# Kernel optimization log

Measured on AMD Instinct MI355X. Metric: run time of the kernel, lower is better.

The kernel has to match this reference:

```python
import jax, jax.numpy as jnp
import numpy as np

NEG_SLOPE = 0.1
K = 3  # kernel_size

def lrelu(x):
    return jnp.where(x >= 0, x, NEG_SLOPE * x)

def setup_inputs() -> dict:
    key = jax.random.key(0)
    ks = jax.random.split(key, 10)
    B, C, H, W = 16, 64, 128, 128
    DEG, RED = 512, 8
    s = 0.02
    return {
        "feat": jax.random.normal(ks[0], (B, C, H, W), jnp.float32),
        "deg": jax.random.normal(ks[1], (B, DEG, 8, 8), jnp.float32),
        # adaptive_size: Linear(deg_fsize -> C), no bias; torch weight [out,in]
        "W_size": jax.random.normal(ks[2], (C, DEG), jnp.float32) * s,
        # kernel net: Linear(C -> C//red), Linear(C//red -> C*K*K)
        "W_k1": jax.random.normal(ks[3], (C // RED, C), jnp.float32) * s,
        "W_k2": jax.random.normal(ks[4], (C * K * K, C // RED), jnp.float32) * s,
        # 1x1 conv C_in -> C_out with bias (stored as [out,in])
        "W_conv": jax.random.normal(ks[5], (C, C), jnp.float32) * s,
        "b_conv": jax.random.normal(ks[6], (C,), jnp.float32) * s,
        # CA layer: 1x1 conv deg_fsize -> C, then C -> C//red -> C
        "W_ac": jax.random.normal(ks[7], (C, DEG), jnp.float32) * s,
        "W_du1": jax.random.normal(ks[8], (C // RED, C), jnp.float32) * s,
        "W_du2": jax.random.normal(ks[9], (C, C // RED), jnp.float32) * s,
    }

def reference(feat, deg, W_size, W_k1, W_k2, W_conv, b_conv, W_ac, W_du1, W_du2):
    b, c, h, w = feat.shape
    # degradation pooled to a vector: AdaptiveAvgPool2d((1,1)) == mean over HW
    dvec = deg.mean(axis=(2, 3))                      # [B, deg_fsize]
    f = dvec @ W_size.T                               # [B, C]
    # per-sample dynamic depthwise kernels
    kern = lrelu(f @ W_k1.T) @ W_k2.T                 # [B, C*K*K]
    kern = kern.reshape(b * c, 1, K, K)               # [B*C, 1, K, K]
    out = jax.lax.conv_general_dilated(
        feat.reshape(1, b * c, h, w), kern,
        window_strides=(1, 1), padding=[((K - 1) // 2,) * 2] * 2,
        feature_group_count=b * c,
        dimension_numbers=("NCHW", "OIHW", "NCHW"))
    out = lrelu(out).reshape(b, c, h, w)
    # trailing 1x1 conv with bias
    out = jnp.einsum("bchw,oc->bohw", out, W_conv) + b_conv[None, :, None, None]
    # CA branch
    fa = dvec @ W_ac.T                                # [B, C]
    att = jax.nn.sigmoid(lrelu(fa @ W_du1.T) @ W_du2.T)  # [B, C_out]
    return out + feat * att[:, :, None, None]
```

## Files before the change

### kernel.cpp

```cpp
#include <hip/hip_runtime.h>
#include <math.h>

#define NEG_SLOPE 0.1f

typedef __attribute__((ext_vector_type(8))) short short8;
typedef __attribute__((ext_vector_type(4))) short short4v;
typedef __attribute__((ext_vector_type(4))) float floatx4;

__device__ __forceinline__ float lrelu(float x) { return x >= 0.0f ? x : NEG_SLOPE * x; }

__device__ __forceinline__ unsigned short f2bf(float x) {
  unsigned u = __float_as_uint(x);
  return (unsigned short)((u + 0x7fffu + ((u >> 16) & 1u)) >> 16);
}

__device__ __forceinline__ float wave_sum64(float v) {
  #pragma unroll
  for (int s = 32; s > 0; s >>= 1) v += __shfl_xor(v, s, 64);
  return v;
}

__global__ __launch_bounds__(256) void prep_dvec(
    const float* __restrict__ deg, float* __restrict__ dvec_ws) {
  const int b = blockIdx.x >> 2;
  const int quarter = blockIdx.x & 3;
  const int t = threadIdx.x;
  const int half = t & 1, row = t >> 1;
  const int d = quarter * 128 + row;
  const float* p = deg + (size_t)b * 32768 + (size_t)d * 64 + half * 32;
  float4 x0 = *(const float4*)(p);
  float4 x1 = *(const float4*)(p + 4);
  float4 x2 = *(const float4*)(p + 8);
  float4 x3 = *(const float4*)(p + 12);
  float4 x4 = *(const float4*)(p + 16);
  float4 x5 = *(const float4*)(p + 20);
  float4 x6 = *(const float4*)(p + 24);
  float4 x7 = *(const float4*)(p + 28);
  float s = (x0.x + x0.y + x0.z + x0.w) + (x1.x + x1.y + x1.z + x1.w) +
            (x2.x + x2.y + x2.z + x2.w) + (x3.x + x3.y + x3.z + x3.w) +
            (x4.x + x4.y + x4.z + x4.w) + (x5.x + x5.y + x5.z + x5.w) +
            (x6.x + x6.y + x6.z + x6.w) + (x7.x + x7.y + x7.z + x7.w);
  s += __shfl_xor(s, 1, 64);
  if (half == 0) dvec_ws[b * 512 + d] = s * (1.0f / 64.0f);
}

__global__ __launch_bounds__(256) void prep_fmul(
    const float* __restrict__ W_size, const float* __restrict__ W_ac,
    const float* __restrict__ dvec_ws, float* __restrict__ f_ws,
    float* __restrict__ fa_ws) {
  const int b = blockIdx.x >> 3;
  const int g = blockIdx.x & 7;
  const int t = threadIdx.x;
  const int dot = t >> 4;
  const int s = t & 15;
  const int c = g * 8 + (dot & 7);
  const float* wr =
      (dot < 8 ? W_size + (size_t)c * 512 : W_ac + (size_t)c * 512) + s * 32;
  const float* dv = dvec_ws + b * 512 + s * 32;
  float p = 0.0f;
  #pragma unroll
  for (int k = 0; k < 8; ++k) {
    float4 w4 = *(const float4*)(wr + k * 4);
    float4 d4 = *(const float4*)(dv + k * 4);
    p += w4.x * d4.x + w4.y * d4.y + w4.z * d4.z + w4.w * d4.w;
  }
  p += __shfl_xor(p, 1, 64);
  p += __shfl_xor(p, 2, 64);
  p += __shfl_xor(p, 4, 64);
  p += __shfl_xor(p, 8, 64);
  if (s == 0) {
    if (dot < 8) f_ws[b * 64 + c] = p;
    else         fa_ws[b * 64 + c] = p;
  }
}

__global__ __launch_bounds__(256) void prep_tail(
    const float* __restrict__ W_k1, const float* __restrict__ W_k2,
    const float* __restrict__ W_du1, const float* __restrict__ W_du2,
    const float* __restrict__ f_ws, const float* __restrict__ fa_ws,
    float* __restrict__ kern_ws, float* __restrict__ att_ws) {
  const int b = blockIdx.x;
  const int t = threadIdx.x;
  __shared__ float t1s[8], t2s[8];
  const int wave = t >> 6, lane = t & 63;
  if (wave == 0) {
    float v = f_ws[b * 64 + lane];
    #pragma unroll
    for (int rr = 0; rr < 8; ++rr) {
      float p = wave_sum64(v * W_k1[rr * 64 + lane]);
      if (lane == 0) t1s[rr] = lrelu(p);
    }
  } else if (wave == 1) {
    float v = fa_ws[b * 64 + lane];
    #pragma unroll
    for (int rr = 0; rr < 8; ++rr) {
      float p = wave_sum64(v * W_du1[rr * 64 + lane]);
      if (lane == 0) t2s[rr] = lrelu(p);
    }
  }
  __syncthreads();

  for (int i = t; i < 576; i += 256) {
    float4 wa0 = *(const float4*)&W_k2[i * 8];
    float4 wa1 = *(const float4*)&W_k2[i * 8 + 4];
    kern_ws[b * 576 + i] =
        t1s[0] * wa0.x + t1s[1] * wa0.y + t1s[2] * wa0.z + t1s[3] * wa0.w +
        t1s[4] * wa1.x + t1s[5] * wa1.y + t1s[6] * wa1.z + t1s[7] * wa1.w;
  }
  if (t < 64) {
    float4 wa0 = *(const float4*)&W_du2[t * 8];
    float4 wa1 = *(const float4*)&W_du2[t * 8 + 4];
    float s = t2s[0] * wa0.x + t2s[1] * wa0.y + t2s[2] * wa0.z + t2s[3] * wa0.w +
              t2s[4] * wa1.x + t2s[5] * wa1.y + t2s[6] * wa1.z + t2s[7] * wa1.w;
    att_ws[b * 64 + t] = 1.0f / (1.0f + expf(-s));
  }
}

__global__ __launch_bounds__(256, 5) void fused_kernel(
    const float* __restrict__ feat, const float* __restrict__ W_conv,
    const float* __restrict__ b_conv, const float* __restrict__ kern_ws,
    const float* __restrict__ att_ws, float* __restrict__ out) {
  const int bid = blockIdx.x;
  const int b = bid >> 7;
  const int h = bid & 127;

  const int t = threadIdx.x;

  __shared__ __align__(16) unsigned short zT[128 * 72];
  __shared__ __align__(16) unsigned short wt[64 * 72];
  __shared__ float ks[576];
  __shared__ float atts[64];
  __shared__ float bcs[64];

  {
    const int o = t >> 2;
    const int c0 = (t & 3) * 16;
    const float* wp = W_conv + o * 64 + c0;
    float4 a0 = *(const float4*)(wp);
    float4 a1 = *(const float4*)(wp + 4);
    float4 a2 = *(const float4*)(wp + 8);
    float4 a3 = *(const float4*)(wp + 12);
    const int sw = ((o >> 2) ^ (o >> 5)) & 7;
    short8 p0, p1;
    p0[0] = f2bf(a0.x); p0[1] = f2bf(a0.y); p0[2] = f2bf(a0.z); p0[3] = f2bf(a0.w);
    p0[4] = f2bf(a1.x); p0[5] = f2bf(a1.y); p0[6] = f2bf(a1.z); p0[7] = f2bf(a1.w);
    p1[0] = f2bf(a2.x); p1[1] = f2bf(a2.y); p1[2] = f2bf(a2.z); p1[3] = f2bf(a2.w);
    p1[4] = f2bf(a3.x); p1[5] = f2bf(a3.y); p1[6] = f2bf(a3.z); p1[7] = f2bf(a3.w);
    const int kc0 = ((c0 >> 3) + 0) ^ sw;
    const int kc1 = ((c0 >> 3) + 1) ^ sw;
    *(short8*)&wt[o * 72 + kc0 * 8] = p0;
    *(short8*)&wt[o * 72 + kc1 * 8] = p1;
  }
  for (int i = t; i < 576; i += 256) ks[i] = kern_ws[b * 576 + i];
  if (t < 64) { atts[t] = att_ws[b * 64 + t]; bcs[t] = b_conv[t]; }
  __syncthreads();

  const size_t base_b = (size_t)b * 64 * 128 * 128;
  const int lane = t & 63, wave = t >> 6;
  const int cq = t >> 5;
  const int gg = t & 31;
  const int w0 = gg * 4;
  const int swz = (gg ^ (gg >> 3)) & 7;
  const float4 zf4 = {0.f, 0.f, 0.f, 0.f};

  const bool hgt0 = (h > 0), hlt = (h < 127);
  const float* fbase = feat + base_b + (size_t)h * 128 + w0;

  #pragma unroll
  for (int it = 0; it < 2; ++it) {
    const int c0 = cq * 4 + it * 32;
    float4 top[4], mid[4], bot[4];
    #pragma unroll
    for (int j = 0; j < 4; ++j) {
      const float* p = fbase + (size_t)(c0 + j) * 16384;
      mid[j] = *(const float4*)p;
      top[j] = hgt0 ? *(const float4*)(p - 128) : zf4;
      bot[j] = hlt  ? *(const float4*)(p + 128) : zf4;
    }
    unsigned short sres[4][4];
    #pragma unroll
    for (int j = 0; j < 4; ++j) {
      const float* kv = &ks[(c0 + j) * 9];
      const float k0 = kv[0], k1 = kv[1], k2 = kv[2];
      const float k3 = kv[3], k4 = kv[4], k5 = kv[5];
      const float k6 = kv[6], k7 = kv[7], k8 = kv[8];
      float a0 = 0.f, a1 = 0.f, a2 = 0.f, a3 = 0.f;
      {
        float4 m = top[j];
        float lf = __shfl(m.w, lane - 1, 64); if (gg == 0)  lf = 0.f;
        float rt = __shfl(m.x, lane + 1, 64); if (gg == 31) rt = 0.f;
        a0 += k0 * lf  + k1 * m.x + k2 * m.y;
        a1 += k0 * m.x + k1 * m.y + k2 * m.z;
        a2 += k0 * m.y + k1 * m.z + k2 * m.w;
        a3 += k0 * m.z + k1 * m.w + k2 * rt;
      }
      {
        float4 m = mid[j];
        float lf = __shfl(m.w, lane - 1, 64); if (gg == 0)  lf = 0.f;
        float rt = __shfl(m.x, lane + 1, 64); if (gg == 31) rt = 0.f;
        a0 += k3 * lf  + k4 * m.x + k5 * m.y;
        a1 += k3 * m.x + k4 * m.y + k5 * m.z;
        a2 += k3 * m.y + k4 * m.z + k5 * m.w;
        a3 += k3 * m.z + k4 * m.w + k5 * rt;
      }
      {
        float4 m = bot[j];
        float lf = __shfl(m.w, lane - 1, 64); if (gg == 0)  lf = 0.f;
        float rt = __shfl(m.x, lane + 1, 64); if (gg == 31) rt = 0.f;
        a0 += k6 * lf  + k7 * m.x + k8 * m.y;
        a1 += k6 * m.x + k7 * m.y + k8 * m.z;
        a2 += k6 * m.y + k7 * m.z + k8 * m.w;
        a3 += k6 * m.z + k7 * m.w + k8 * rt;
      }
      sres[j][0] = f2bf(lrelu(a0));
      sres[j][1] = f2bf(lrelu(a1));
      sres[j][2] = f2bf(lrelu(a2));
      sres[j][3] = f2bf(lrelu(a3));
    }
    const int chunk = (cq >> 1) + it * 4;
    const int kcs = ((chunk ^ swz) * 8) + (cq & 1) * 4;
    #pragma unroll
    for (int i = 0; i < 4; ++i) {
      short4v sv;
      sv[0] = (short)sres[0][i]; sv[1] = (short)sres[1][i];
      sv[2] = (short)sres[2][i]; sv[3] = (short)sres[3][i];
      *(short4v*)&zT[(w0 + i) * 72 + kcs] = sv;
    }
  }
  __syncthreads();

  {
    const int r = lane & 15, q = lane >> 4;

    short8 az[2][2];
    #pragma unroll
    for (int wm2 = 0; wm2 < 2; ++wm2) {
      const int w = (wave * 2 + wm2) * 16 + r;
      const int sz = ((w >> 2) ^ (w >> 5)) & 7;
      #pragma unroll
      for (int ksp = 0; ksp < 2; ++ksp) {
        const int kc = (ksp * 4 + q) ^ sz;
        az[wm2][ksp] = *(const short8*)&zT[w * 72 + kc * 8];
      }
    }
    short8 bw[4][2];
    #pragma unroll
    for (int nt = 0; nt < 4; ++nt) {
      const int o = nt * 16 + r;
      const int so = ((o >> 2) ^ (o >> 5)) & 7;
      #pragma unroll
      for (int ksp = 0; ksp < 2; ++ksp) {
        const int kc = (ksp * 4 + q) ^ so;
        bw[nt][ksp] = *(const short8*)&wt[o * 72 + kc * 8];
      }
    }

    floatx4 acc[2][4];
    #pragma unroll
    for (int wm2 = 0; wm2 < 2; ++wm2)
      #pragma unroll
      for (int nt = 0; nt < 4; ++nt) acc[wm2][nt] = (floatx4){0.f, 0.f, 0.f, 0.f};

    #pragma unroll
    for (int wm2 = 0; wm2 < 2; ++wm2)
      #pragma unroll
      for (int nt = 0; nt < 4; ++nt)
        #pragma unroll
        for (int ksp = 0; ksp < 2; ++ksp)
          acc[wm2][nt] = __builtin_amdgcn_mfma_f32_16x16x32_bf16(
              az[wm2][ksp], bw[nt][ksp], acc[wm2][nt], 0, 0, 0);

    #pragma unroll
    for (int wm2 = 0; wm2 < 2; ++wm2) {
      const int wb = (wave * 2 + wm2) * 16 + q * 4;
      #pragma unroll
      for (int nt = 0; nt < 4; ++nt) {
        const int o = nt * 16 + r;
        const size_t off = base_b + (size_t)o * 16384 + (size_t)h * 128 + wb;
        float4 fv = *(const float4*)(feat + off);
        const float at = atts[o], bo = bcs[o];
        floatx4 a = acc[wm2][nt];
        float4 ov;
        ov.x = a[0] + bo + at * fv.x;
        ov.y = a[1] + bo + at * fv.y;
        ov.z = a[2] + bo + at * fv.z;
        ov.w = a[3] + bo + at * fv.w;
        *(float4*)(out + off) = ov;
      }
    }
  }
}

extern "C" void kernel_launch(void* const* d_in, const int* in_sizes, int n_in,
                              void* d_out, int out_size, void* d_ws, size_t ws_size,
                              hipStream_t stream) {
  const float* feat   = (const float*)d_in[0];
  const float* deg    = (const float*)d_in[1];
  const float* W_size = (const float*)d_in[2];
  const float* W_k1   = (const float*)d_in[3];
  const float* W_k2   = (const float*)d_in[4];
  const float* W_conv = (const float*)d_in[5];
  const float* b_conv = (const float*)d_in[6];
  const float* W_ac   = (const float*)d_in[7];
  const float* W_du1  = (const float*)d_in[8];
  const float* W_du2  = (const float*)d_in[9];
  float* out = (float*)d_out;

  float* kern_ws = (float*)d_ws;
  float* att_ws  = kern_ws + 16 * 576;
  float* dvec_ws = att_ws + 16 * 64;
  float* f_ws    = dvec_ws + 16 * 512;
  float* fa_ws   = f_ws + 16 * 64;

  prep_dvec<<<64, 256, 0, stream>>>(deg, dvec_ws);
  prep_fmul<<<128, 256, 0, stream>>>(W_size, W_ac, dvec_ws, f_ws, fa_ws);
  prep_tail<<<16, 256, 0, stream>>>(W_k1, W_k2, W_du1, W_du2, f_ws, fa_ws,
                                    kern_ws, att_ws);
  fused_kernel<<<2048, 256, 0, stream>>>(feat, W_conv, b_conv, kern_ws, att_ws,
                                         out);
}
```

Before: 175.8 us.

## Precompute bf16 conv weights once and read B fragments from global memory

```diff
diff --git a/kernel.cpp b/kernel.cpp
--- a/kernel.cpp
+++ b/kernel.cpp
@@ -18,6 +18,23 @@
   #pragma unroll
   for (int s = 32; s > 0; s >>= 1) v += __shfl_xor(v, s, 64);
   return v;
+}
+
+__global__ __launch_bounds__(256) void prep_wconv(
+    const float* __restrict__ W_conv, unsigned short* __restrict__ wcb) {
+  const int t = threadIdx.x;
+  const float* p = W_conv + t * 16;
+  float4 a0 = *(const float4*)(p);
+  float4 a1 = *(const float4*)(p + 4);
+  float4 a2 = *(const float4*)(p + 8);
+  float4 a3 = *(const float4*)(p + 12);
+  short8 p0, p1;
+  p0[0] = f2bf(a0.x); p0[1] = f2bf(a0.y); p0[2] = f2bf(a0.z); p0[3] = f2bf(a0.w);
+  p0[4] = f2bf(a1.x); p0[5] = f2bf(a1.y); p0[6] = f2bf(a1.z); p0[7] = f2bf(a1.w);
+  p1[0] = f2bf(a2.x); p1[1] = f2bf(a2.y); p1[2] = f2bf(a2.z); p1[3] = f2bf(a2.w);
+  p1[4] = f2bf(a3.x); p1[5] = f2bf(a3.y); p1[6] = f2bf(a3.z); p1[7] = f2bf(a3.w);
+  *(short8*)&wcb[t * 16] = p0;
+  *(short8*)&wcb[t * 16 + 8] = p1;
 }
 
 __global__ __launch_bounds__(256) void prep_dvec(
@@ -116,41 +133,22 @@
   }
 }
 
-__global__ __launch_bounds__(256, 5) void fused_kernel(
-    const float* __restrict__ feat, const float* __restrict__ W_conv,
+__global__ __launch_bounds__(256, 6) void fused_kernel(
+    const float* __restrict__ feat, const unsigned short* __restrict__ wcb,
     const float* __restrict__ b_conv, const float* __restrict__ kern_ws,
     const float* __restrict__ att_ws, float* __restrict__ out) {
   const int bid = blockIdx.x;
-  const int b = bid >> 7;
-  const int h = bid & 127;
+  const int wg = ((bid & 7) << 8) + (bid >> 3);
+  const int b = wg >> 7;
+  const int h = wg & 127;
 
   const int t = threadIdx.x;
 
   __shared__ __align__(16) unsigned short zT[128 * 72];
-  __shared__ __align__(16) unsigned short wt[64 * 72];
   __shared__ float ks[576];
   __shared__ float atts[64];
   __shared__ float bcs[64];
 
-  {
-    const int o = t >> 2;
-    const int c0 = (t & 3) * 16;
-    const float* wp = W_conv + o * 64 + c0;
-    float4 a0 = *(const float4*)(wp);
-    float4 a1 = *(const float4*)(wp + 4);
-    float4 a2 = *(const float4*)(wp + 8);
-    float4 a3 = *(const float4*)(wp + 12);
-    const int sw = ((o >> 2) ^ (o >> 5)) & 7;
-    short8 p0, p1;
-    p0[0] = f2bf(a0.x); p0[1] = f2bf(a0.y); p0[2] = f2bf(a0.z); p0[3] = f2bf(a0.w);
-    p0[4] = f2bf(a1.x); p0[5] = f2bf(a1.y); p0[6] = f2bf(a1.z); p0[7] = f2bf(a1.w);
-    p1[0] = f2bf(a2.x); p1[1] = f2bf(a2.y); p1[2] = f2bf(a2.z); p1[3] = f2bf(a2.w);
-    p1[4] = f2bf(a3.x); p1[5] = f2bf(a3.y); p1[6] = f2bf(a3.z); p1[7] = f2bf(a3.w);
-    const int kc0 = ((c0 >> 3) + 0) ^ sw;
-    const int kc1 = ((c0 >> 3) + 1) ^ sw;
-    *(short8*)&wt[o * 72 + kc0 * 8] = p0;
-    *(short8*)&wt[o * 72 + kc1 * 8] = p1;
-  }
   for (int i = t; i < 576; i += 256) ks[i] = kern_ws[b * 576 + i];
   if (t < 64) { atts[t] = att_ws[b * 64 + t]; bcs[t] = b_conv[t]; }
   __syncthreads();
@@ -247,12 +245,9 @@
     #pragma unroll
     for (int nt = 0; nt < 4; ++nt) {
       const int o = nt * 16 + r;
-      const int so = ((o >> 2) ^ (o >> 5)) & 7;
-      #pragma unroll
-      for (int ksp = 0; ksp < 2; ++ksp) {
-        const int kc = (ksp * 4 + q) ^ so;
-        bw[nt][ksp] = *(const short8*)&wt[o * 72 + kc * 8];
-      }
+      #pragma unroll
+      for (int ksp = 0; ksp < 2; ++ksp)
+        bw[nt][ksp] = *(const short8*)&wcb[o * 64 + ksp * 32 + q * 8];
     }
 
     floatx4 acc[2][4];
@@ -311,11 +306,13 @@
   float* dvec_ws = att_ws + 16 * 64;
   float* f_ws    = dvec_ws + 16 * 512;
   float* fa_ws   = f_ws + 16 * 64;
-
+  unsigned short* wcb = (unsigned short*)(fa_ws + 16 * 64);
+
+  prep_wconv<<<1, 256, 0, stream>>>(W_conv, wcb);
   prep_dvec<<<64, 256, 0, stream>>>(deg, dvec_ws);
   prep_fmul<<<128, 256, 0, stream>>>(W_size, W_ac, dvec_ws, f_ws, fa_ws);
   prep_tail<<<16, 256, 0, stream>>>(W_k1, W_k2, W_du1, W_du2, f_ws, fa_ws,
                                     kern_ws, att_ws);
-  fused_kernel<<<2048, 256, 0, stream>>>(feat, W_conv, b_conv, kern_ws, att_ws,
+  fused_kernel<<<2048, 256, 0, stream>>>(feat, wcb, b_conv, kern_ws, att_ws,
                                          out);
 }
```

Result: slower. 196.5 us (+11.8%).
